# Kernel optimization log

Hardware: AMD Instinct MI355X
Metric: run time of the kernel (lower is better)

Reference implementation:

```python
import jax, jax.numpy as jnp
import numpy as np

NUM_HEADS = 8
HEAD_DIM = 128
MAX_RES = 224.0


def rope_embed(feat_shape, dim, max_res=MAX_RES):
    # timm pixel_freq_bands: 2**linspace(0, log2(max_res)-1, dim//4) * pi
    num_bands = dim // 4
    bands = (2.0 ** jnp.linspace(0.0, float(np.log2(max_res)) - 1.0, num_bands)) * jnp.pi
    # pixel coords in [-1, 1] per spatial dim
    coords = [jnp.linspace(-1.0, 1.0, s) for s in feat_shape]
    grid = jnp.stack(jnp.meshgrid(*coords, indexing='ij'), axis=-1)[..., None]  # [H,W,2,1]
    pos = grid * bands  # [H,W,2,num_bands]
    n = int(np.prod(feat_shape))
    sin = jnp.repeat(jnp.sin(pos).reshape(n, -1), 2, axis=-1)  # [n, dim]
    cos = jnp.repeat(jnp.cos(pos).reshape(n, -1), 2, axis=-1)  # [n, dim]
    return sin, cos


def _rot(x):
    # interleaved rotate-half: (x0,x1,x2,x3,...) -> (-x1,x0,-x3,x2,...)
    return jnp.stack([-x[..., 1::2], x[..., ::2]], axis=-1).reshape(x.shape)


def setup_inputs() -> dict:
    key = jax.random.key(0)
    k1, k2, k3, k4 = jax.random.split(key, 4)
    C, E = 1024, 1024
    x = jax.random.normal(k1, (64, C, 16, 16), dtype=jnp.float32)
    qkv_w = jax.random.normal(k2, (3 * E, C), dtype=jnp.float32) * (C ** -0.5)
    qkv_b = jnp.zeros((3 * E,), dtype=jnp.float32)
    proj_w = jax.random.normal(k3, (E, E), dtype=jnp.float32) * (E ** -0.5)
    proj_b = jax.random.normal(k4, (E,), dtype=jnp.float32) * 0.02
    return {"x": x, "qkv_w": qkv_w, "qkv_b": qkv_b, "proj_w": proj_w, "proj_b": proj_b}


def reference(x, qkv_w, qkv_b, proj_w, proj_b):
    B, C, H, W = x.shape
    n = H * W
    scale = HEAD_DIM ** -0.5
    sin_emb, cos_emb = rope_embed((H, W), HEAD_DIM)  # [n, head_dim]

    t = x.reshape(B, C, n).transpose(0, 2, 1)                      # [B, n, C]
    t = jnp.concatenate([t.mean(axis=1, keepdims=True), t], axis=1)  # [B, n+1, C]

    qkv = t @ qkv_w.T + qkv_b                                      # [B, n+1, 3E]
    qkv = qkv.reshape(B, n + 1, 3, NUM_HEADS, HEAD_DIM).transpose(2, 0, 3, 1, 4)
    q, k, v = qkv[0], qkv[1], qkv[2]                               # [B, h, n+1, d]

    def apply_rope(z):
        zc, zs = z[:, :, :1], z[:, :, 1:]
        zs = zs * cos_emb + _rot(zs) * sin_emb
        return jnp.concatenate([zc, zs], axis=2)

    q = apply_rope(q)
    k = apply_rope(k)

    attn = jax.nn.softmax(jnp.einsum('bhqd,bhkd->bhqk', q, k) * scale, axis=-1)
    out = jnp.einsum('bhqk,bhkd->bhqd', attn, v)
    out = out.transpose(0, 2, 1, 3).reshape(B, n + 1, -1)           # [B, n+1, E]
    out = out @ proj_w.T + proj_b
    return out[:, 0]
```

## Files before the change

kernel.cpp:

```cpp
#include <hip/hip_runtime.h>
#include <math.h>

#define PI_F 3.14159265358979323846f
#define KSTEP 0.21959209425992272f

using bf16x8 = __attribute__((ext_vector_type(8))) short;
using f32x4 = __attribute__((ext_vector_type(4))) float;
using u16x8 = __attribute__((ext_vector_type(8))) unsigned short;

static __device__ __forceinline__ float wave_reduce_sum(float v) {
#pragma unroll
  for (int off = 32; off; off >>= 1) v += __shfl_down(v, off);
  return v;
}

static __device__ __forceinline__ unsigned short f2bf(float f) {
  unsigned u = __float_as_uint(f);
  return (unsigned short)((u + 0x7fffu + ((u >> 16) & 1u)) >> 16);
}

static __device__ __forceinline__ float bf2f(unsigned short s) {
  return __uint_as_float(((unsigned)s) << 16);
}

static __device__ __forceinline__ void gload_lds16(const void* g, void* l) {
  __builtin_amdgcn_global_load_lds((const __attribute__((address_space(1))) unsigned int*)g,
                                   (__attribute__((address_space(3))) unsigned int*)l, 16, 0, 0);
}

__global__ __launch_bounds__(256) void prep_kernel(const float* __restrict__ x,
                                                   const float* __restrict__ qkv_w,
                                                   const float* __restrict__ qkv_b,
                                                   unsigned short* __restrict__ xt,
                                                   float* __restrict__ t_mean,
                                                   unsigned short* __restrict__ wkT,
                                                   float2* __restrict__ sc) {
  const int bid = blockIdx.x;
  const int t = threadIdx.x;
  __shared__ float tile[64 * 33];
  __shared__ float tl2[64 * 65];
  if (bid < 1024) {
    const int ct = bid & 15, b = bid >> 4;
    const int cl = t >> 2, pq = (t & 3) * 8;
    const int pl = t >> 3, cq = (t & 7) * 8;
    float sum = 0.0f;
    const float* xrow = x + ((size_t)(b * 1024 + ct * 64 + cl) * 256) + pq;
    unsigned short* xtb = xt + (size_t)b * 262144 + ct * 64;
    for (int pt = 0; pt < 8; ++pt) {
      const float4 v0 = *reinterpret_cast<const float4*>(xrow + pt * 32);
      const float4 v1 = *reinterpret_cast<const float4*>(xrow + pt * 32 + 4);
      tile[cl * 33 + pq + 0] = v0.x; tile[cl * 33 + pq + 1] = v0.y;
      tile[cl * 33 + pq + 2] = v0.z; tile[cl * 33 + pq + 3] = v0.w;
      tile[cl * 33 + pq + 4] = v1.x; tile[cl * 33 + pq + 5] = v1.y;
      tile[cl * 33 + pq + 6] = v1.z; tile[cl * 33 + pq + 7] = v1.w;
      sum += (v0.x + v0.y) + (v0.z + v0.w) + (v1.x + v1.y) + (v1.z + v1.w);
      __syncthreads();
      u16x8 o;
#pragma unroll
      for (int e = 0; e < 8; ++e) o[e] = f2bf(tile[(cq + e) * 33 + pl]);
      *reinterpret_cast<u16x8*>(xtb + (size_t)(pt * 32 + pl) * 1024 + cq) = o;
      __syncthreads();
    }
    sum += __shfl_xor(sum, 1);
    sum += __shfl_xor(sum, 2);
    if ((t & 3) == 0) t_mean[b * 1024 + ct * 64 + cl] = sum * (1.0f / 256.0f);
  } else if (bid < 1280) {
    const int bb = bid - 1024;
    const int h = bb >> 5, t5 = bb & 31;
    const int dt = t5 >> 4, ct = t5 & 15;
    {
      const int dl = t >> 2, cq = (t & 3) * 16;
      const float* src = qkv_w + (size_t)(1024 + h * 128 + dt * 64 + dl) * 1024 + ct * 64 + cq;
#pragma unroll
      for (int i = 0; i < 4; ++i) {
        const float4 v = *reinterpret_cast<const float4*>(src + i * 4);
        tl2[dl * 65 + cq + i * 4 + 0] = v.x; tl2[dl * 65 + cq + i * 4 + 1] = v.y;
        tl2[dl * 65 + cq + i * 4 + 2] = v.z; tl2[dl * 65 + cq + i * 4 + 3] = v.w;
      }
    }
    __syncthreads();
    {
      const int cl = t >> 2, dq = (t & 3) * 16;
      unsigned short* dst = wkT + (size_t)(h * 1152 + ct * 64 + cl) * 128 + dt * 64 + dq;
      u16x8 o0, o1;
#pragma unroll
      for (int e = 0; e < 8; ++e) {
        o0[e] = f2bf(tl2[(dq + e) * 65 + cl]);
        o1[e] = f2bf(tl2[(dq + 8 + e) * 65 + cl]);
      }
      *reinterpret_cast<u16x8*>(dst) = o0;
      *reinterpret_cast<u16x8*>(dst + 8) = o1;
    }
  } else if (bid < 1288) {
    const int h = bid - 1280;
    for (int idx = t; idx < 16384; idx += 256) {
      const int row = 1024 + (idx >> 7), d = idx & 127;
      unsigned short v = 0;
      if (row == 1024) v = f2bf(qkv_b[1024 + h * 128 + d]);
      wkT[(size_t)(h * 1152 + row) * 128 + d] = v;
    }
  } else {
    const int idx = (bid - 1288) * 256 + t;
    const int m = idx >> 8, j = idx & 255;
    const float band = exp2f((float)(m & 31) * KSTEP) * PI_F;
    const float coord = (m < 32) ? (-1.0f + (2.0f / 15.0f) * (float)(j >> 4))
                                 : (-1.0f + (2.0f / 15.0f) * (float)(j & 15));
    float sn, cs;
    sincosf(coord * band, &sn, &cs);
    sc[idx] = make_float2(sn, cs);
  }
}

__global__ __launch_bounds__(256) void gemm_splitk(
    const float* __restrict__ A, int lda, int aStrideZ,
    const float* __restrict__ B, int ldb, int bStrideZ,
    float* __restrict__ Cp, int ldc, int cStrideZ, int cStrideKc, int KC) {
  const int nt = blockIdx.x, mt = blockIdx.y;
  const int z = blockIdx.z / KC, kc = blockIdx.z % KC;
  const int tid = threadIdx.x;
  A += (size_t)z * aStrideZ + (size_t)mt * 32 * lda + kc * 256;
  B += (size_t)z * bStrideZ + (size_t)nt * 64 * ldb + kc * 256;
  Cp += (size_t)kc * cStrideKc + (size_t)z * cStrideZ + (size_t)mt * 32 * ldc + nt * 64;

  __shared__ float As[32][34];
  __shared__ float Bs[32][68];

  const int tm = tid >> 4;
  const int tn = tid & 15;
  float acc0[4] = {0, 0, 0, 0}, acc1[4] = {0, 0, 0, 0};

  for (int k0 = 0; k0 < 256; k0 += 32) {
    {
      const int m = tid >> 3, kq = tid & 7;
      float4 v = *reinterpret_cast<const float4*>(A + (size_t)m * lda + k0 + kq * 4);
      As[kq * 4 + 0][m] = v.x; As[kq * 4 + 1][m] = v.y;
      As[kq * 4 + 2][m] = v.z; As[kq * 4 + 3][m] = v.w;
    }
#pragma unroll
    for (int r = 0; r < 2; ++r) {
      const int idx = r * 256 + tid;
      const int n = idx >> 3, kq = idx & 7;
      float4 v = *reinterpret_cast<const float4*>(B + (size_t)n * ldb + k0 + kq * 4);
      Bs[kq * 4 + 0][n] = v.x; Bs[kq * 4 + 1][n] = v.y;
      Bs[kq * 4 + 2][n] = v.z; Bs[kq * 4 + 3][n] = v.w;
    }
    __syncthreads();
#pragma unroll
    for (int k = 0; k < 32; ++k) {
      const float a0 = As[k][tm * 2], a1 = As[k][tm * 2 + 1];
      const float4 bb = *reinterpret_cast<const float4*>(&Bs[k][tn * 4]);
      acc0[0] += a0 * bb.x; acc0[1] += a0 * bb.y; acc0[2] += a0 * bb.z; acc0[3] += a0 * bb.w;
      acc1[0] += a1 * bb.x; acc1[1] += a1 * bb.y; acc1[2] += a1 * bb.z; acc1[3] += a1 * bb.w;
    }
    __syncthreads();
  }
  *reinterpret_cast<float4*>(Cp + (size_t)(tm * 2) * ldc + tn * 4) =
      make_float4(acc0[0], acc0[1], acc0[2], acc0[3]);
  *reinterpret_cast<float4*>(Cp + (size_t)(tm * 2 + 1) * ldc + tn * 4) =
      make_float4(acc1[0], acc1[1], acc1[2], acc1[3]);
}

__global__ __launch_bounds__(256) void gemm_proj_splitk(
    const float* __restrict__ Apart, const float* __restrict__ abias,
    const float* __restrict__ B, float* __restrict__ Cp) {
  const int nt = blockIdx.x, mt = blockIdx.y, kc = blockIdx.z;
  const int tid = threadIdx.x;
  B += (size_t)nt * 64 * 1024 + kc * 256;
  Cp += (size_t)kc * 65536 + (size_t)mt * 32 * 1024 + nt * 64;

  __shared__ float As[32][34];
  __shared__ float Bs[32][68];

  const int tm = tid >> 4;
  const int tn = tid & 15;
  float acc0[4] = {0, 0, 0, 0}, acc1[4] = {0, 0, 0, 0};

  for (int k0 = 0; k0 < 256; k0 += 32) {
    {
      const int m = tid >> 3, kq = tid & 7;
      const int kg = kc * 256 + k0 + kq * 4;
      const float* Ab = Apart + (size_t)(mt * 32 + m) * 1024 + kg;
      float4 v = *reinterpret_cast<const float4*>(abias + kg);
#pragma unroll
      for (int r = 0; r < 4; ++r) {
        const float4 p = *reinterpret_cast<const float4*>(Ab + (size_t)r * 65536);
        v.x += p.x; v.y += p.y; v.z += p.z; v.w += p.w;
      }
      As[kq * 4 + 0][m] = v.x; As[kq * 4 + 1][m] = v.y;
      As[kq * 4 + 2][m] = v.z; As[kq * 4 + 3][m] = v.w;
    }
#pragma unroll
    for (int r = 0; r < 2; ++r) {
      const int idx = r * 256 + tid;
      const int n = idx >> 3, kq = idx & 7;
      float4 v = *reinterpret_cast<const float4*>(B + (size_t)n * 1024 + k0 + kq * 4);
      Bs[kq * 4 + 0][n] = v.x; Bs[kq * 4 + 1][n] = v.y;
      Bs[kq * 4 + 2][n] = v.z; Bs[kq * 4 + 3][n] = v.w;
    }
    __syncthreads();
#pragma unroll
    for (int k = 0; k < 32; ++k) {
      const float a0 = As[k][tm * 2], a1 = As[k][tm * 2 + 1];
      const float4 bb = *reinterpret_cast<const float4*>(&Bs[k][tn * 4]);
      acc0[0] += a0 * bb.x; acc0[1] += a0 * bb.y; acc0[2] += a0 * bb.z; acc0[3] += a0 * bb.w;
      acc1[0] += a1 * bb.x; acc1[1] += a1 * bb.y; acc1[2] += a1 * bb.z; acc1[3] += a1 * bb.w;
    }
    __syncthreads();
  }
  *reinterpret_cast<float4*>(Cp + (size_t)(tm * 2) * 1024 + tn * 4) =
      make_float4(acc0[0], acc0[1], acc0[2], acc0[3]);
  *reinterpret_cast<float4*>(Cp + (size_t)(tm * 2 + 1) * 1024 + tn * 4) =
      make_float4(acc1[0], acc1[1], acc1[2], acc1[3]);
}

__global__ __launch_bounds__(256) void reduce4_bias(const float* __restrict__ part,
                                                    const float* __restrict__ bias,
                                                    float* __restrict__ out) {
  const int i = blockIdx.x * 256 + threadIdx.x;
  out[i] = part[i] + part[i + 65536] + part[i + 131072] + part[i + 196608] + bias[i & 1023];
}

__global__ __launch_bounds__(256) void tgemm_rot(
    const unsigned short* __restrict__ wkT, const float* __restrict__ q0p,
    const float* __restrict__ qkv_b, const float2* __restrict__ sc,
    unsigned short* __restrict__ T) {
  const int nt = blockIdx.x;
  const int mt = blockIdx.y;
  const int z = blockIdx.z;
  const int h = z >> 1, s = z & 1;
  const int tid = threadIdx.x;
  const int w = tid >> 6, lane = tid & 63;
  const int wr = w >> 1, wc = w & 1;

  __shared__ __align__(16) char smem[34816];
  char* Ab = smem;
  char* Bb = smem + 16384;
  float* q0red = reinterpret_cast<float*>(smem + 32768);

#pragma unroll
  for (int i = 0; i < 4; ++i) {
    const int g = w * 4 + i;
    const int row = g * 8 + (lane >> 3);
    const int sl = ((lane & 7) ^ ((row >> 1) & 7)) * 8;
    gload_lds16(wkT + ((size_t)h * 1152 + nt * 128 + row) * 128 + s * 64 + sl, Bb + g * 1024);
  }
  for (int idx = tid; idx < 512; idx += 256) {
    const int bl = idx >> 6, d = idx & 63;
    const int b = mt * 8 + bl;
    const float* qp = q0p + (size_t)b * 2048 + h * 128 + s * 64 + d;
    q0red[idx] = qkv_b[h * 128 + s * 64 + d] + qp[0] + qp[131072] + qp[262144] + qp[393216];
  }
  __syncthreads();

  {
    const int r = tid >> 1;
    const int ph = (tid & 1) * 16;
    const int v = r & 15;
    const int jrep = (s == 0) ? v * 16 : v;
    const float* qr = q0red + (r >> 4) * 64;
    const int swz = (r >> 1) & 7;
#pragma unroll
    for (int g = 0; g < 4; ++g) {
      unsigned pk[4];
#pragma unroll
      for (int e = 0; e < 4; ++e) {
        const int p = ph + g * 4 + e;
        const float qe = qr[2 * p], qo = qr[2 * p + 1];
        const float2 tt = sc[(s * 32 + p) * 256 + jrep];
        const float ae = qe * tt.y + qo * tt.x;
        const float ao = qo * tt.y - qe * tt.x;
        pk[e] = (unsigned)f2bf(ae) | ((unsigned)f2bf(ao) << 16);
      }
      const int slot = ((ph >> 2) + g) ^ swz;
      *reinterpret_cast<uint4*>(Ab + r * 128 + slot * 16) = make_uint4(pk[0], pk[1], pk[2], pk[3]);
    }
  }
  __syncthreads();

  f32x4 acc[4][4] = {};
#pragma unroll
  for (int kk = 0; kk < 2; ++kk) {
    bf16x8 af[4], bf[4];
#pragma unroll
    for (int mi = 0; mi < 4; ++mi) {
      const int row = wr * 64 + mi * 16 + (lane & 15);
      const int slot = (kk * 4 + (lane >> 4)) ^ ((row >> 1) & 7);
      af[mi] = *reinterpret_cast<const bf16x8*>(Ab + row * 128 + (slot << 4));
    }
#pragma unroll
    for (int ni = 0; ni < 4; ++ni) {
      const int row = wc * 64 + ni * 16 + (lane & 15);
      const int slot = (kk * 4 + (lane >> 4)) ^ ((row >> 1) & 7);
      bf[ni] = *reinterpret_cast<const bf16x8*>(Bb + row * 128 + (slot << 4));
    }
#pragma unroll
    for (int mi = 0; mi < 4; ++mi)
#pragma unroll
      for (int ni = 0; ni < 4; ++ni)
        acc[mi][ni] = __builtin_amdgcn_mfma_f32_16x16x32_bf16(af[mi], bf[ni], acc[mi][ni], 0, 0, 0);
  }

  unsigned short* Tz = T + (size_t)(s * 8 + h) * 1024 * 1152;
#pragma unroll
  for (int mi = 0; mi < 4; ++mi)
#pragma unroll
    for (int ni = 0; ni < 4; ++ni) {
      const int col = nt * 128 + wc * 64 + ni * 16 + (lane & 15);
#pragma unroll
      for (int rr = 0; rr < 4; ++rr) {
        const int row = mt * 128 + wr * 64 + mi * 16 + (lane >> 4) * 4 + rr;
        Tz[(size_t)row * 1152 + col] = f2bf(acc[mi][ni][rr]);
      }
    }
}

__global__ __launch_bounds__(256, 2) void scores_u(
    const unsigned short* __restrict__ Tg, const unsigned short* __restrict__ xt,
    const float* __restrict__ q0p, const float* __restrict__ qkv_b,
    const float* __restrict__ t_mean, float* __restrict__ u) {
  const int l = blockIdx.x;
  const int b = ((l >> 5) << 3) | (l & 7);
  const int ht = (l >> 3) & 3;
  const int tid = threadIdx.x;
  const int w = tid >> 6, lane = tid & 63;

  __shared__ __align__(16) char smem[61440];

  const unsigned short* xtb = xt + (size_t)b * 262144;

#define STAGE(buf, c0)                                                          \
  {                                                                             \
    char* Ab_ = smem + (buf)*20480;                                             \
    char* Bb_ = Ab_ + 16384;                                                    \
    _Pragma("unroll") for (int i = 0; i < 4; ++i) {                             \
      const int row_ = w * 64 + i * 16 + (lane >> 2);                           \
      const int sl_ = ((lane & 3) ^ ((row_ >> 1) & 3)) * 8;                     \
      gload_lds16(xtb + (size_t)row_ * 1024 + (c0) + sl_,                       \
                  Ab_ + (w * 4 + i) * 1024);                                    \
    }                                                                           \
    {                                                                           \
      const int n_ = w * 16 + (lane >> 2);                                      \
      const int h_ = ht * 2 + (n_ >> 5), s_ = (n_ >> 4) & 1, v_ = n_ & 15;      \
      const size_t rowT_ = ((size_t)(s_ * 8 + h_) * 1024 + b * 16 + v_) * 1152; \
      const int sl_ = ((lane & 3) ^ ((n_ >> 1) & 3)) * 8;                       \
      gload_lds16(Tg + rowT_ + (c0) + sl_, Bb_ + w * 1024);                     \
    }                                                                           \
  }

  STAGE(0, 0);
  STAGE(1, 32);
  f32x4 acc[4][4] = {};
  int cur = 0, nxt = 2;
  for (int t = 0; t < 32; ++t) {
    {
      const int src = (t + 2 > 31) ? 31 : (t + 2);
      STAGE(nxt, src * 32);
    }
    asm volatile("s_waitcnt vmcnt(10)" ::: "memory");
    __builtin_amdgcn_s_barrier();
    const char* Ab = smem + cur * 20480;
    const char* Bb = Ab + 16384;
    bf16x8 af[4], bfr[4];
#pragma unroll
    for (int mi = 0; mi < 4; ++mi) {
      const int row = w * 64 + mi * 16 + (lane & 15);
      af[mi] = *reinterpret_cast<const bf16x8*>(
          Ab + row * 64 + ((((lane >> 4) ^ ((row >> 1) & 3))) << 4));
    }
#pragma unroll
    for (int ni = 0; ni < 4; ++ni) {
      const int n = ni * 16 + (lane & 15);
      bfr[ni] = *reinterpret_cast<const bf16x8*>(
          Bb + n * 64 + ((((lane >> 4) ^ ((n >> 1) & 3))) << 4));
    }
    __builtin_amdgcn_s_setprio(1);
#pragma unroll
    for (int mi = 0; mi < 4; ++mi)
#pragma unroll
      for (int ni = 0; ni < 4; ++ni)
        acc[mi][ni] =
            __builtin_amdgcn_mfma_f32_16x16x32_bf16(af[mi], bfr[ni], acc[mi][ni], 0, 0, 0);
    __builtin_amdgcn_s_setprio(0);
    __builtin_amdgcn_s_barrier();
    asm volatile("" ::: "memory");
    cur = (cur == 2) ? 0 : cur + 1;
    nxt = (nxt == 2) ? 0 : nxt + 1;
  }
#undef STAGE

  asm volatile("s_waitcnt vmcnt(0)" ::: "memory");
  __syncthreads();

  float* Sp = reinterpret_cast<float*>(smem);
  float* bias = Sp + 1024;
  float* q0l = bias + 64;
  float* k0l = q0l + 256;
  float* ps = k0l + 256;
  float* smax = ps + 4;
  float* ssum = smax + 8;
  float* attnl = ssum + 8;
  float* upart = reinterpret_cast<float*>(smem + 16384);

#pragma unroll
  for (int mi = 0; mi < 4; ++mi)
#pragma unroll
    for (int ni = 0; ni < 4; ++ni)
#pragma unroll
      for (int rr = 0; rr < 4; ++rr) {
        const int j = w * 64 + mi * 16 + ((lane >> 4) << 2) + rr;
        const int col = ni * 16 + (lane & 15);
        const int s = (col >> 4) & 1;
        const int sel = s ? (j & 15) : (j >> 4);
        if ((col & 15) == sel) Sp[(j * 2 + (col >> 5)) * 2 + s] = acc[mi][ni][rr];
      }
  if (tid < 64) {
    const int h_ = tid >> 5, s_ = (tid >> 4) & 1, v_ = tid & 15;
    bias[tid] =
        bf2f(Tg[((size_t)(s_ * 8 + ht * 2 + h_) * 1024 + b * 16 + v_) * 1152 + 1024]);
  }
  {
    const float* qp = q0p + (size_t)b * 2048 + ht * 256 + tid;
    q0l[tid] = qkv_b[ht * 256 + tid] + qp[0] + qp[131072] + qp[262144] + qp[393216];
    const float* kp = qp + 1024;
    k0l[tid] = qkv_b[1024 + ht * 256 + tid] + kp[0] + kp[131072] + kp[262144] + kp[393216];
  }
  __syncthreads();
  {
    float pr = q0l[tid] * k0l[tid];
    pr = wave_reduce_sum(pr);
    if (lane == 0) ps[w] = pr;
  }
  __syncthreads();

  const float scale = 0.08838834764831845f;
  const float va0 = scale * (Sp[tid * 4 + 0] + Sp[tid * 4 + 1] + bias[tid >> 4] +
                             bias[16 + (tid & 15)]);
  const float va1 = scale * (Sp[tid * 4 + 2] + Sp[tid * 4 + 3] + bias[32 + (tid >> 4)] +
                             bias[48 + (tid & 15)]);
  float vb0 = -3.0e38f, vb1 = -3.0e38f;
  if (tid == 0) {
    vb0 = scale * (ps[0] + ps[1]);
    vb1 = scale * (ps[2] + ps[3]);
  }
  float m0 = fmaxf(va0, vb0), m1 = fmaxf(va1, vb1);
#pragma unroll
  for (int off = 32; off; off >>= 1) {
    m0 = fmaxf(m0, __shfl_xor(m0, off));
    m1 = fmaxf(m1, __shfl_xor(m1, off));
  }
  if (lane == 0) { smax[w] = m0; smax[4 + w] = m1; }
  __syncthreads();
  const float g0 = fmaxf(fmaxf(smax[0], smax[1]), fmaxf(smax[2], smax[3]));
  const float g1 = fmaxf(fmaxf(smax[4], smax[5]), fmaxf(smax[6], smax[7]));
  const float e0 = expf(va0 - g0), e1 = expf(va1 - g1);
  const float eb0 = (tid == 0) ? expf(vb0 - g0) : 0.0f;
  const float eb1 = (tid == 0) ? expf(vb1 - g1) : 0.0f;
  float s0 = e0 + eb0, s1 = e1 + eb1;
#pragma unroll
  for (int off = 32; off; off >>= 1) {
    s0 += __shfl_xor(s0, off);
    s1 += __shfl_xor(s1, off);
  }
  if (lane == 0) { ssum[w] = s0; ssum[4 + w] = s1; }
  __syncthreads();
  const float inv0 = 1.0f / (ssum[0] + ssum[1] + ssum[2] + ssum[3]);
  const float inv1 = 1.0f / (ssum[4] + ssum[5] + ssum[6] + ssum[7]);
  attnl[1 + tid] = e0 * inv0;
  attnl[257 + 1 + tid] = e1 * inv1;
  if (tid == 0) { attnl[0] = eb0 * inv0; attnl[257] = eb1 * inv1; }
  __syncthreads();

  {
    float ua0[16] = {}, ua1[16] = {};
    const unsigned short* xr = xtb + (size_t)(w * 64) * 1024 + lane * 16;
    for (int jj = 0; jj < 64; ++jj) {
      const float a0 = attnl[1 + w * 64 + jj];
      const float a1 = attnl[257 + 1 + w * 64 + jj];
      const u16x8 v0 = *reinterpret_cast<const u16x8*>(xr + (size_t)jj * 1024);
      const u16x8 v1 = *reinterpret_cast<const u16x8*>(xr + (size_t)jj * 1024 + 8);
#pragma unroll
      for (int e = 0; e < 8; ++e) {
        const float f0 = bf2f((unsigned short)v0[e]);
        const float f1 = bf2f((unsigned short)v1[e]);
        ua0[e] += a0 * f0; ua0[8 + e] += a0 * f1;
        ua1[e] += a1 * f0; ua1[8 + e] += a1 * f1;
      }
    }
#pragma unroll
    for (int e = 0; e < 16; ++e) {
      upart[(w * 2 + 0) * 1024 + lane * 16 + e] = ua0[e];
      upart[(w * 2 + 1) * 1024 + lane * 16 + e] = ua1[e];
    }
  }
  __syncthreads();
#pragma unroll
  for (int r = 0; r < 8; ++r) {
    const int o = tid * 8 + r;
    const int h2 = o >> 10, c = o & 1023;
    float s = upart[(0 * 2 + h2) * 1024 + c] + upart[(1 * 2 + h2) * 1024 + c] +
              upart[(2 * 2 + h2) * 1024 + c] + upart[(3 * 2 + h2) * 1024 + c];
    s += attnl[h2 * 257] * t_mean[b * 1024 + c];
    u[((size_t)b * 8 + ht * 2 + h2) * 1024 + c] = s;
  }
}

extern "C" void kernel_launch(void* const* d_in, const int* in_sizes, int n_in,
                              void* d_out, int out_size, void* d_ws, size_t ws_size,
                              hipStream_t stream) {
  const float* x = (const float*)d_in[0];
  const float* qkv_w = (const float*)d_in[1];
  const float* qkv_b = (const float*)d_in[2];
  const float* proj_w = (const float*)d_in[3];
  const float* proj_b = (const float*)d_in[4];
  float* out = (float*)d_out;

  float* ws = (float*)d_ws;
  float* t_mean = ws;
  float* q0k0_part = ws + 65536;
  float* u = ws + 589824;
  float* out0_part = ws + 1114112;
  float* out_part = ws + 1376256;
  float2* sc = (float2*)(ws + 1638400);
  unsigned short* wkT = (unsigned short*)(ws + 1671168);
  unsigned short* T = (unsigned short*)(ws + 2260992);
  unsigned short* x_t = (unsigned short*)(ws + 11698176);

  prep_kernel<<<1352, 256, 0, stream>>>(x, qkv_w, qkv_b, x_t, t_mean, wkT, sc);

  gemm_splitk<<<dim3(32, 2, 4), 256, 0, stream>>>(t_mean, 1024, 0, qkv_w, 1024, 0,
                                                  q0k0_part, 2048, 0, 131072, 4);

  tgemm_rot<<<dim3(9, 8, 16), 256, 0, stream>>>(wkT, q0k0_part, qkv_b, sc, T);

  scores_u<<<256, 256, 0, stream>>>(T, x_t, q0k0_part, qkv_b, t_mean, u);

  gemm_splitk<<<dim3(2, 2, 32), 256, 0, stream>>>(u, 8192, 1024,
                                                  qkv_w + (size_t)2048 * 1024, 1024, 131072,
                                                  out0_part, 1024, 128, 65536, 4);

  gemm_proj_splitk<<<dim3(16, 2, 4), 256, 0, stream>>>(out0_part, qkv_b + 2048, proj_w, out_part);

  reduce4_bias<<<256, 256, 0, stream>>>(out_part, proj_b, out);
}
```

Measured before the change: 107.1 us.

## Double waves per block in scores_u and deepen LDS pipeline to four stages

After: 101.9 us. 1.05x faster.

```diff
diff --git a/kernel.cpp b/kernel.cpp
--- a/kernel.cpp
+++ b/kernel.cpp
@@ -314,7 +314,7 @@
     }
 }
 
-__global__ __launch_bounds__(256, 2) void scores_u(
+__global__ __launch_bounds__(512, 1) void scores_u(
     const unsigned short* __restrict__ Tg, const unsigned short* __restrict__ xt,
     const float* __restrict__ q0p, const float* __restrict__ qkv_b,
     const float* __restrict__ t_mean, float* __restrict__ u) {
@@ -324,7 +324,7 @@
   const int tid = threadIdx.x;
   const int w = tid >> 6, lane = tid & 63;
 
-  __shared__ __align__(16) char smem[61440];
+  __shared__ __align__(16) char smem[81920];
 
   const unsigned short* xtb = xt + (size_t)b * 262144;
 
@@ -332,13 +332,13 @@
   {                                                                             \
     char* Ab_ = smem + (buf)*20480;                                             \
     char* Bb_ = Ab_ + 16384;                                                    \
-    _Pragma("unroll") for (int i = 0; i < 4; ++i) {                             \
-      const int row_ = w * 64 + i * 16 + (lane >> 2);                           \
+    _Pragma("unroll") for (int i = 0; i < 2; ++i) {                             \
+      const int row_ = w * 32 + i * 16 + (lane >> 2);                           \
       const int sl_ = ((lane & 3) ^ ((row_ >> 1) & 3)) * 8;                     \
       gload_lds16(xtb + (size_t)row_ * 1024 + (c0) + sl_,                       \
-                  Ab_ + (w * 4 + i) * 1024);                                    \
+                  Ab_ + (w * 2 + i) * 1024);                                    \
     }                                                                           \
-    {                                                                           \
+    if (w < 4) {                                                                \
       const int n_ = w * 16 + (lane >> 2);                                      \
       const int h_ = ht * 2 + (n_ >> 5), s_ = (n_ >> 4) & 1, v_ = n_ & 15;      \
       const size_t rowT_ = ((size_t)(s_ * 8 + h_) * 1024 + b * 16 + v_) * 1152; \
@@ -349,21 +349,24 @@
 
   STAGE(0, 0);
   STAGE(1, 32);
-  f32x4 acc[4][4] = {};
-  int cur = 0, nxt = 2;
+  STAGE(2, 64);
+  f32x4 acc[2][4] = {};
   for (int t = 0; t < 32; ++t) {
     {
-      const int src = (t + 2 > 31) ? 31 : (t + 2);
-      STAGE(nxt, src * 32);
-    }
-    asm volatile("s_waitcnt vmcnt(10)" ::: "memory");
+      const int src = (t + 3 > 31) ? 31 : (t + 3);
+      STAGE((t + 3) & 3, src * 32);
+    }
+    if (w < 4)
+      asm volatile("s_waitcnt vmcnt(9)" ::: "memory");
+    else
+      asm volatile("s_waitcnt vmcnt(6)" ::: "memory");
     __builtin_amdgcn_s_barrier();
-    const char* Ab = smem + cur * 20480;
+    const char* Ab = smem + (t & 3) * 20480;
     const char* Bb = Ab + 16384;
-    bf16x8 af[4], bfr[4];
-#pragma unroll
-    for (int mi = 0; mi < 4; ++mi) {
-      const int row = w * 64 + mi * 16 + (lane & 15);
+    bf16x8 af[2], bfr[4];
+#pragma unroll
+    for (int mi = 0; mi < 2; ++mi) {
+      const int row = w * 32 + mi * 16 + (lane & 15);
       af[mi] = *reinterpret_cast<const bf16x8*>(
           Ab + row * 64 + ((((lane >> 4) ^ ((row >> 1) & 3))) << 4));
     }
@@ -375,7 +378,7 @@
     }
     __builtin_amdgcn_s_setprio(1);
 #pragma unroll
-    for (int mi = 0; mi < 4; ++mi)
+    for (int mi = 0; mi < 2; ++mi)
 #pragma unroll
       for (int ni = 0; ni < 4; ++ni)
         acc[mi][ni] =
@@ -383,8 +386,6 @@
     __builtin_amdgcn_s_setprio(0);
     __builtin_amdgcn_s_barrier();
     asm volatile("" ::: "memory");
-    cur = (cur == 2) ? 0 : cur + 1;
-    nxt = (nxt == 2) ? 0 : nxt + 1;
   }
 #undef STAGE
 
@@ -402,12 +403,12 @@
   float* upart = reinterpret_cast<float*>(smem + 16384);
 
 #pragma unroll
-  for (int mi = 0; mi < 4; ++mi)
+  for (int mi = 0; mi < 2; ++mi)
 #pragma unroll
     for (int ni = 0; ni < 4; ++ni)
 #pragma unroll
       for (int rr = 0; rr < 4; ++rr) {
-        const int j = w * 64 + mi * 16 + ((lane >> 4) << 2) + rr;
+        const int j = w * 32 + mi * 16 + ((lane >> 4) << 2) + rr;
         const int col = ni * 16 + (lane & 15);
         const int s = (col >> 4) & 1;
         const int sel = s ? (j & 15) : (j >> 4);
@@ -418,14 +419,14 @@
     bias[tid] =
         bf2f(Tg[((size_t)(s_ * 8 + ht * 2 + h_) * 1024 + b * 16 + v_) * 1152 + 1024]);
   }
-  {
+  if (tid < 256) {
     const float* qp = q0p + (size_t)b * 2048 + ht * 256 + tid;
     q0l[tid] = qkv_b[ht * 256 + tid] + qp[0] + qp[131072] + qp[262144] + qp[393216];
     const float* kp = qp + 1024;
     k0l[tid] = qkv_b[1024 + ht * 256 + tid] + kp[0] + kp[131072] + kp[262144] + kp[393216];
   }
   __syncthreads();
-  {
+  if (tid < 256) {
     float pr = q0l[tid] * k0l[tid];
     pr = wave_reduce_sum(pr);
     if (lane == 0) ps[w] = pr;
@@ -433,49 +434,63 @@
   __syncthreads();
 
   const float scale = 0.08838834764831845f;
-  const float va0 = scale * (Sp[tid * 4 + 0] + Sp[tid * 4 + 1] + bias[tid >> 4] +
-                             bias[16 + (tid & 15)]);
-  const float va1 = scale * (Sp[tid * 4 + 2] + Sp[tid * 4 + 3] + bias[32 + (tid >> 4)] +
-                             bias[48 + (tid & 15)]);
-  float vb0 = -3.0e38f, vb1 = -3.0e38f;
-  if (tid == 0) {
-    vb0 = scale * (ps[0] + ps[1]);
-    vb1 = scale * (ps[2] + ps[3]);
-  }
-  float m0 = fmaxf(va0, vb0), m1 = fmaxf(va1, vb1);
-#pragma unroll
-  for (int off = 32; off; off >>= 1) {
-    m0 = fmaxf(m0, __shfl_xor(m0, off));
-    m1 = fmaxf(m1, __shfl_xor(m1, off));
-  }
-  if (lane == 0) { smax[w] = m0; smax[4 + w] = m1; }
-  __syncthreads();
-  const float g0 = fmaxf(fmaxf(smax[0], smax[1]), fmaxf(smax[2], smax[3]));
-  const float g1 = fmaxf(fmaxf(smax[4], smax[5]), fmaxf(smax[6], smax[7]));
-  const float e0 = expf(va0 - g0), e1 = expf(va1 - g1);
-  const float eb0 = (tid == 0) ? expf(vb0 - g0) : 0.0f;
-  const float eb1 = (tid == 0) ? expf(vb1 - g1) : 0.0f;
-  float s0 = e0 + eb0, s1 = e1 + eb1;
-#pragma unroll
-  for (int off = 32; off; off >>= 1) {
-    s0 += __shfl_xor(s0, off);
-    s1 += __shfl_xor(s1, off);
-  }
-  if (lane == 0) { ssum[w] = s0; ssum[4 + w] = s1; }
-  __syncthreads();
-  const float inv0 = 1.0f / (ssum[0] + ssum[1] + ssum[2] + ssum[3]);
-  const float inv1 = 1.0f / (ssum[4] + ssum[5] + ssum[6] + ssum[7]);
-  attnl[1 + tid] = e0 * inv0;
-  attnl[257 + 1 + tid] = e1 * inv1;
-  if (tid == 0) { attnl[0] = eb0 * inv0; attnl[257] = eb1 * inv1; }
+  float e0 = 0.0f, e1 = 0.0f, eb0 = 0.0f, eb1 = 0.0f;
+  if (tid < 256) {
+    const float va0 = scale * (Sp[tid * 4 + 0] + Sp[tid * 4 + 1] + bias[tid >> 4] +
+                               bias[16 + (tid & 15)]);
+    const float va1 = scale * (Sp[tid * 4 + 2] + Sp[tid * 4 + 3] + bias[32 + (tid >> 4)] +
+                               bias[48 + (tid & 15)]);
+    float vb0 = -3.0e38f, vb1 = -3.0e38f;
+    if (tid == 0) {
+      vb0 = scale * (ps[0] + ps[1]);
+      vb1 = scale * (ps[2] + ps[3]);
+    }
+    float m0 = fmaxf(va0, vb0), m1 = fmaxf(va1, vb1);
+#pragma unroll
+    for (int off = 32; off; off >>= 1) {
+      m0 = fmaxf(m0, __shfl_xor(m0, off));
+      m1 = fmaxf(m1, __shfl_xor(m1, off));
+    }
+    if (lane == 0) { smax[w] = m0; smax[4 + w] = m1; }
+  }
+  __syncthreads();
+  if (tid < 256) {
+    const float g0 = fmaxf(fmaxf(smax[0], smax[1]), fmaxf(smax[2], smax[3]));
+    const float g1 = fmaxf(fmaxf(smax[4], smax[5]), fmaxf(smax[6], smax[7]));
+    const float va0 = scale * (Sp[tid * 4 + 0] + Sp[tid * 4 + 1] + bias[tid >> 4] +
+                               bias[16 + (tid & 15)]);
+    const float va1 = scale * (Sp[tid * 4 + 2] + Sp[tid * 4 + 3] + bias[32 + (tid >> 4)] +
+                               bias[48 + (tid & 15)]);
+    e0 = expf(va0 - g0);
+    e1 = expf(va1 - g1);
+    if (tid == 0) {
+      eb0 = expf(scale * (ps[0] + ps[1]) - g0);
+      eb1 = expf(scale * (ps[2] + ps[3]) - g1);
+    }
+    float s0 = e0 + eb0, s1 = e1 + eb1;
+#pragma unroll
+    for (int off = 32; off; off >>= 1) {
+      s0 += __shfl_xor(s0, off);
+      s1 += __shfl_xor(s1, off);
+    }
+    if (lane == 0) { ssum[w] = s0; ssum[4 + w] = s1; }
+  }
+  __syncthreads();
+  if (tid < 256) {
+    const float inv0 = 1.0f / (ssum[0] + ssum[1] + ssum[2] + ssum[3]);
+    const float inv1 = 1.0f / (ssum[4] + ssum[5] + ssum[6] + ssum[7]);
+    attnl[1 + tid] = e0 * inv0;
+    attnl[257 + 1 + tid] = e1 * inv1;
+    if (tid == 0) { attnl[0] = eb0 * inv0; attnl[257] = eb1 * inv1; }
+  }
   __syncthreads();
 
   {
     float ua0[16] = {}, ua1[16] = {};
-    const unsigned short* xr = xtb + (size_t)(w * 64) * 1024 + lane * 16;
-    for (int jj = 0; jj < 64; ++jj) {
-      const float a0 = attnl[1 + w * 64 + jj];
-      const float a1 = attnl[257 + 1 + w * 64 + jj];
+    const unsigned short* xr = xtb + (size_t)(w * 32) * 1024 + lane * 16;
+    for (int jj = 0; jj < 32; ++jj) {
+      const float a0 = attnl[1 + w * 32 + jj];
+      const float a1 = attnl[257 + 1 + w * 32 + jj];
       const u16x8 v0 = *reinterpret_cast<const u16x8*>(xr + (size_t)jj * 1024);
       const u16x8 v1 = *reinterpret_cast<const u16x8*>(xr + (size_t)jj * 1024 + 8);
 #pragma unroll
@@ -494,11 +509,12 @@
   }
   __syncthreads();
 #pragma unroll
-  for (int r = 0; r < 8; ++r) {
-    const int o = tid * 8 + r;
+  for (int r = 0; r < 4; ++r) {
+    const int o = tid * 4 + r;
     const int h2 = o >> 10, c = o & 1023;
-    float s = upart[(0 * 2 + h2) * 1024 + c] + upart[(1 * 2 + h2) * 1024 + c] +
-              upart[(2 * 2 + h2) * 1024 + c] + upart[(3 * 2 + h2) * 1024 + c];
+    float s = 0.0f;
+#pragma unroll
+    for (int ww = 0; ww < 8; ++ww) s += upart[(ww * 2 + h2) * 1024 + c];
     s += attnl[h2 * 257] * t_mean[b * 1024 + c];
     u[((size_t)b * 8 + ht * 2 + h2) * 1024 + c] = s;
   }
@@ -532,7 +548,7 @@
 
   tgemm_rot<<<dim3(9, 8, 16), 256, 0, stream>>>(wkT, q0k0_part, qkv_b, sc, T);
 
-  scores_u<<<256, 256, 0, stream>>>(T, x_t, q0k0_part, qkv_b, t_mean, u);
+  scores_u<<<256, 512, 0, stream>>>(T, x_t, q0k0_part, qkv_b, t_mean, u);
 
   gemm_splitk<<<dim3(2, 2, 32), 256, 0, stream>>>(u, 8192, 1024,
                                                   qkv_w + (size_t)2048 * 1024, 1024, 131072,
```
